# Performance work log

Measured on AMD Instinct MI355X. Metric: run time of the kernel, lower is better.

## Reference

```python
import jax, jax.numpy as jnp
import numpy as np

BS, D_HID, D_EMB, N_LABELS = 8192, 1024, 256, 64
EPS = 1e-8  # torch cosine_similarity norm clamp


def _l2norm(x):
    return x / jnp.maximum(jnp.linalg.norm(x, axis=-1, keepdims=True), EPS)


def setup_inputs() -> dict:
    key = jax.random.key(0)
    k1, k2, k3, k4 = jax.random.split(key, 4)
    return {
        "mask_emb": jax.random.normal(k1, (BS, D_HID), dtype=jnp.float32),
        "W": jax.random.normal(k2, (D_EMB, D_HID), dtype=jnp.float32) * 0.02,
        "b": jnp.zeros((D_EMB,), dtype=jnp.float32),
        "label_emb": jax.random.normal(k3, (N_LABELS, D_EMB), dtype=jnp.float32),
        "labels": jax.random.randint(k4, (BS,), 0, N_LABELS, dtype=jnp.int64 if jax.config.jax_enable_x64 else jnp.int32),
    }


def reference(mask_emb, W, b, label_emb, labels):
    bs = mask_emb.shape[0]
    emb = mask_emb @ W.T + b                      # [bs, E] transform_matrix
    en = _l2norm(emb)                              # normalized sample embeddings
    ln = _l2norm(label_emb)                        # normalized prototypes

    S = en @ en.T                                  # [bs, bs] pairwise cosine sim
    C = en @ ln.T                                  # [bs, L]  sample-vs-prototype cosine sim

    same = labels[:, None] == labels[None, :]      # [bs, bs]
    eye = jnp.eye(bs, dtype=bool)
    offdiag = ~eye

    # ---- inter-sample loss ----
    # N[i] = sum over negatives (different label) of exp(S[i,k]); constant over j
    expS = jnp.exp(S)
    N = jnp.sum(jnp.where(~same, expS, 0.0), axis=1)          # [bs]
    # pos_loss is S[i,j] for same-label j!=i, else 0
    P = jnp.where(same & offdiag, S, 0.0)                      # [bs, bs]
    terms = -P + jnp.log(N[:, None] + jnp.exp(P))
    inter = jnp.sum(jnp.where(offdiag, terms, 0.0)) / (bs * bs)

    # ---- sample-prototype losses ----
    pos = jnp.take_along_axis(C, labels[:, None], axis=1)[:, 0]   # C[i, labels[i]]
    onehot = jax.nn.one_hot(labels, label_emb.shape[0], dtype=C.dtype)
    expC = jnp.exp(C)
    neg1 = jnp.sum(expC * (1.0 - onehot), axis=1)                 # sum over other prototypes
    # neg2[i] = sum_{j: labels[j]!=labels[i]} exp(cos(label_emb[labels[i]], emb[j])) = exp(C[j, labels[i]])
    M = expC.T[labels]                                            # [bs, bs], M[i,j] = exp(C[j, labels[i]])
    neg2 = jnp.sum(jnp.where(~same, M, 0.0), axis=1)              # 0 if no negatives -> log(exp(pos)) = pos
    exp_pos = jnp.exp(pos)
    proto1 = jnp.mean(-pos + jnp.log(neg1 + exp_pos))
    proto2 = jnp.mean(-pos + jnp.log(neg2 + exp_pos))

    a1, a2 = 0.5, 0.5
    return a1 * inter + a2 * (proto1 + proto2)
```

## Files before the change

kernel.cpp:

```cpp
#include <hip/hip_runtime.h>
#include <hip/hip_bf16.h>
#include <math.h>

#define BS 8192
#define DH 1024
#define DE 256
#define NL 64
#define SBST 224

typedef __attribute__((ext_vector_type(8))) short short8;
typedef __attribute__((ext_vector_type(4))) float f32x4;
typedef unsigned short ushort;

__device__ __forceinline__ ushort bf16b(float f){
  unsigned u = __float_as_uint(f);
  unsigned r = (u + 0x7FFFu + ((u >> 16) & 1u)) >> 16;
  return (ushort)r;
}

__device__ __forceinline__ float fexp2(float x){
  float r;
  asm("v_exp_f32 %0, %1" : "=v"(r) : "v"(x));
  return r;
}

__device__ __forceinline__ void gload_lds16(const void* g, void* l){
  __builtin_amdgcn_global_load_lds((const __attribute__((address_space(1))) void*)g,
                                   (__attribute__((address_space(3))) void*)l, 16, 0, 0);
}

__global__ __launch_bounds__(256) void wcvt_kernel(const float* __restrict__ W, ushort* __restrict__ Wb){
  int i = (blockIdx.x*256 + threadIdx.x) * 8;
  float4 v0 = *(const float4*)(W+i);
  float4 v1 = *(const float4*)(W+i+4);
  short8 o;
  o[0]=bf16b(v0.x); o[1]=bf16b(v0.y); o[2]=bf16b(v0.z); o[3]=bf16b(v0.w);
  o[4]=bf16b(v1.x); o[5]=bf16b(v1.y); o[6]=bf16b(v1.z); o[7]=bf16b(v1.w);
  *(short8*)(Wb+i) = o;
}

#define EMB_AB(P) ((ushort*)pool + (P)*2048)
#define EMB_BB(P) ((ushort*)pool + 4096 + (P)*16384)

#define EMB_LOADA(KB) do { \
  va0 = *(const float4*)(aptr + (KB)); \
  va1 = *(const float4*)(aptr + (KB) + 4); \
} while(0)

#define EMB_WRITEA(P) do { \
  short8 o; \
  o[0]=bf16b(va0.x); o[1]=bf16b(va0.y); o[2]=bf16b(va0.z); o[3]=bf16b(va0.w); \
  o[4]=bf16b(va1.x); o[5]=bf16b(va1.y); o[6]=bf16b(va1.z); o[7]=bf16b(va1.w); \
  *(short8*)&EMB_AB(P)[tid*8] = o; \
} while(0)

#define EMB_STAGEB(P, KB) do { \
  _Pragma("unroll") \
  for (int q=0;q<8;q++){ \
    int chunk = q*4 + w; \
    int lin = chunk*64 + lane; \
    int row = lin >> 3, cc = lin & 7; \
    int lc = cc ^ (row & 7); \
    gload_lds16(Wb + (size_t)row*DH + (KB) + lc*8, EMB_BB(P) + chunk*512); \
  } \
} while(0)

#define EMB_COMPUTE(P) do { \
  _Pragma("unroll") \
  for (int kk=0;kk<2;kk++){ \
    short8 af[2], bfr[4]; \
    _Pragma("unroll") \
    for (int m=0;m<2;m++){ \
      int row = m*16 + (lane & 15); \
      int phys = (kk*4 + (lane >> 4)) ^ (row & 7); \
      af[m] = *(const short8*)&EMB_AB(P)[row*64 + phys*8]; \
    } \
    _Pragma("unroll") \
    for (int n=0;n<4;n++){ \
      int row = w*64 + n*16 + (lane & 15); \
      int phys = (kk*4 + (lane >> 4)) ^ (row & 7); \
      bfr[n] = *(const short8*)&EMB_BB(P)[row*64 + phys*8]; \
    } \
    _Pragma("unroll") \
    for (int m=0;m<2;m++) \
      _Pragma("unroll") \
      for (int n=0;n<4;n++) \
        acc[m][n] = __builtin_amdgcn_mfma_f32_16x16x32_bf16(af[m], bfr[n], acc[m][n], 0,0,0); \
  } \
} while(0)

__global__ __launch_bounds__(256) void emb_mega_kernel(const float* __restrict__ mask,
    const ushort* __restrict__ Wb, const float* __restrict__ bias,
    const float* __restrict__ label_emb, ushort* __restrict__ lnb,
    const int* __restrict__ labels, int* __restrict__ cnt,
    int* __restrict__ offs, int* __restrict__ groups,
    ushort* __restrict__ enb, ushort* __restrict__ enb2){
  __shared__ __align__(16) char pool[74368];
  int b = blockIdx.x, tid = threadIdx.x;
  if (b == 0){
    ushort* loc = (ushort*)pool;
    int* off_s = (int*)(pool + 32768);
    int* cnt_s = (int*)(pool + 33032);
    int t = tid;
    #pragma unroll
    for (int l=0;l<64;l++) loc[t*64 + l]=0;
    __syncthreads();
    int base = t * 32;
    for (int i=0;i<32;i++){
      int y = labels[base+i];
      loc[t*64 + y] = (ushort)(loc[t*64 + y] + 1);
    }
    __syncthreads();
    if (t < 64){
      int run = 0;
      for (int tt=0;tt<256;tt++){
        int v = loc[tt*64 + t];
        loc[tt*64 + t] = (ushort)run;
        run += v;
      }
      cnt_s[t] = run;
      cnt[t] = run;
    }
    __syncthreads();
    if (t == 0){
      int acc2 = 0;
      for (int l=0;l<64;l++){ off_s[l] = acc2; acc2 += cnt_s[l]; }
      off_s[64] = acc2;
    }
    __syncthreads();
    if (t < 65) offs[t] = off_s[t];
    for (int i=0;i<32;i++){
      int idx = base + i;
      int y = labels[idx];
      int p = off_s[y] + loc[t*64 + y];
      loc[t*64 + y] = (ushort)(loc[t*64 + y] + 1);
      groups[p] = idx;
    }
    return;
  }
  if (b < 65){
    float* red = (float*)pool;
    int l = b - 1, t = tid;
    float v = label_emb[l*DE + t];
    red[t] = v*v;
    __syncthreads();
    for (int s=128;s>0;s>>=1){
      if (t<s) red[t] += red[t+s];
      __syncthreads();
    }
    float inv = 1.0f / fmaxf(sqrtf(red[0]), 1e-8f);
    lnb[l*DE + t] = bf16b(v * inv);
    return;
  }
  float* sq = (float*)(pool + 73728);
  float* inv_s = (float*)(pool + 74240);
  int lane = tid & 63, w = tid >> 6;
  int rb = (b - 65) * 32;
  int arow = tid >> 3, alc = (tid & 7) ^ (arow & 7);
  const float* aptr = mask + (size_t)(rb + arow)*DH + alc*8;
  float4 va0, va1;
  f32x4 acc[2][4] = {};
  EMB_LOADA(0);
  EMB_WRITEA(0);
  EMB_STAGEB(0, 0);
  __syncthreads();
  int buf = 0;
  for (int kb = 0; kb < 16; kb++){
    if (kb < 15){
      EMB_LOADA((kb+1)*64);
      EMB_STAGEB(buf^1, (kb+1)*64);
    }
    EMB_COMPUTE(buf);
    if (kb < 15) EMB_WRITEA(buf^1);
    __syncthreads();
    buf ^= 1;
  }
  int qr = lane >> 4, c15 = lane & 15;
  float bv[4];
  #pragma unroll
  for (int n=0;n<4;n++) bv[n] = bias[w*64 + n*16 + c15];
  #pragma unroll
  for (int m=0;m<2;m++){
    #pragma unroll
    for (int r=0;r<4;r++){
      float s = 0.f;
      #pragma unroll
      for (int n=0;n<4;n++){
        float v = acc[m][n][r] + bv[n];
        acc[m][n][r] = v;
        s += v*v;
      }
      #pragma unroll
      for (int msk=8; msk>=1; msk>>=1) s += __shfl_xor(s, msk);
      if (c15 == 0) sq[w*32 + m*16 + qr*4 + r] = s;
    }
  }
  __syncthreads();
  if (tid < 32){
    float s = sq[tid] + sq[32+tid] + sq[64+tid] + sq[96+tid];
    inv_s[tid] = 1.0f / fmaxf(sqrtf(s), 1e-8f);
  }
  __syncthreads();
  #pragma unroll
  for (int m=0;m<2;m++){
    #pragma unroll
    for (int r=0;r<4;r++){
      int row = m*16 + qr*4 + r;
      float iv = inv_s[row];
      #pragma unroll
      for (int n=0;n<4;n++){
        int col = w*64 + n*16 + c15;
        float v = acc[m][n][r] * iv;
        enb [(size_t)(rb+row)*DE + col] = bf16b(v);
        enb2[(size_t)(rb+row)*DE + col] = bf16b(v * 1.44269504f);
      }
    }
  }
}

__global__ __launch_bounds__(256, 4) void fused3_kernel(const ushort* __restrict__ enb,
    const ushort* __restrict__ enb2, const ushort* __restrict__ lnb,
    const int* __restrict__ labels, const int* __restrict__ cnt,
    const int* __restrict__ offs, const int* __restrict__ groups,
    float* __restrict__ N_part, float* __restrict__ pos, float* __restrict__ rowsum,
    float* __restrict__ T_part, float* __restrict__ G_part,
    float* __restrict__ samesum, ushort* __restrict__ Sbuf){
  __shared__ __align__(16) char pool[33792];
  int blk = blockIdx.x;
  int tid = threadIdx.x, lane = tid & 63, w = tid >> 6;
  int qr = lane >> 4, c15 = lane & 15;

  if (blk < 128){
    ushort* Ab = (ushort*)pool;
    ushort* Bb = (ushort*)(pool + 8192);
    float* TpS = (float*)(pool + 16384);
    float* GpS = (float*)(pool + 17408);
    int rb = blk * 64;
    f32x4 acc[4] = {};
    for (int kb = 0; kb < DE; kb += 64){
      #pragma unroll
      for (int q=0;q<2;q++){
        int chunk = q*4 + w;
        int lin = chunk*64 + lane;
        int row = lin >> 3, cc = lin & 7;
        int lc = cc ^ (row & 7);
        gload_lds16(enb + (size_t)(rb+row)*DE + kb + lc*8, Ab + chunk*512);
      }
      #pragma unroll
      for (int q=0;q<2;q++){
        int chunk = q*4 + w;
        int lin = chunk*64 + lane;
        int row = lin >> 3, cc = lin & 7;
        int lc = cc ^ (row & 7);
        gload_lds16(lnb + (size_t)row*DE + kb + lc*8, Bb + chunk*512);
      }
      __syncthreads();
      #pragma unroll
      for (int kk=0;kk<2;kk++){
        int arow = w*16 + c15;
        int aphys = (kk*4 + (lane >> 4)) ^ (arow & 7);
        short8 af = *(const short8*)&Ab[arow*64 + aphys*8];
        #pragma unroll
        for (int ni=0;ni<4;ni++){
          int brow = ni*16 + c15;
          int bphys = (kk*4 + (lane >> 4)) ^ (brow & 7);
          short8 bfr = *(const short8*)&Bb[brow*64 + bphys*8];
          acc[ni] = __builtin_amdgcn_mfma_f32_16x16x32_bf16(af, bfr, acc[ni], 0,0,0);
        }
      }
      __syncthreads();
    }
    int yr[4];
    #pragma unroll
    for (int r=0;r<4;r++) yr[r] = labels[rb + w*16 + qr*4 + r];
    float e[4][4];
    #pragma unroll
    for (int ni=0;ni<4;ni++)
      #pragma unroll
      for (int r=0;r<4;r++) e[ni][r] = __expf(acc[ni][r]);
    #pragma unroll
    for (int r=0;r<4;r++){
      float rs = e[0][r]+e[1][r]+e[2][r]+e[3][r];
      float ps = 0.f;
      #pragma unroll
      for (int ni=0;ni<4;ni++) if (ni*16 + c15 == yr[r]) ps = acc[ni][r];
      #pragma unroll
      for (int msk=8; msk>=1; msk>>=1){ rs += __shfl_xor(rs, msk); ps += __shfl_xor(ps, msk); }
      if (c15 == 0){
        int grow = rb + w*16 + qr*4 + r;
        rowsum[grow] = rs;
        pos[grow] = ps;
      }
    }
    #pragma unroll
    for (int ni=0;ni<4;ni++){
      int col = ni*16 + c15;
      float t = 0.f, g = 0.f;
      #pragma unroll
      for (int r=0;r<4;r++){
        t += e[ni][r];
        if (col == yr[r]) g += e[ni][r];
      }
      t += __shfl_xor(t, 16); t += __shfl_xor(t, 32);
      g += __shfl_xor(g, 16); g += __shfl_xor(g, 32);
      if (qr == 0){ TpS[w*64 + col] = t; GpS[w*64 + col] = g; }
    }
    __syncthreads();
    if (tid < 64){
      T_part[(size_t)blk*64 + tid] = TpS[tid]+TpS[64+tid]+TpS[128+tid]+TpS[192+tid];
      G_part[(size_t)blk*64 + tid] = GpS[tid]+GpS[64+tid]+GpS[128+tid]+GpS[192+tid];
    }
    return;
  }

  if (blk < 384){
    ushort* Ab = (ushort*)pool;
    ushort* Bb = (ushort*)(pool + 8192);
    int* aidx = (int*)(pool + 24576);
    int* gidx = (int*)(pool + 24832);
    float* Gs = (float*)(pool + 25344);
    int gid = blk - 128;
    int l = gid & 63, rt = gid >> 6;
    int m = cnt[l], off = offs[l];
    ushort* Sl = Sbuf + (size_t)l * SBST * SBST;
    for (int ra = rt*64; ra < m; ra += 256){
      __syncthreads();
      if (tid < 64){ int a = ra + tid; aidx[tid] = groups[off + (a < m ? a : 0)]; }
      float Ga[4] = {0.f,0.f,0.f,0.f};
      for (int cb2 = 0; cb2 < m; cb2 += 128){
        __syncthreads();
        if (tid < 128){ int bb = cb2 + tid; gidx[tid] = groups[off + (bb < m ? bb : 0)]; }
        __syncthreads();
        f32x4 acc[4][2] = {};
        for (int kb = 0; kb < DE; kb += 64){
          #pragma unroll
          for (int q=0;q<2;q++){
            int chunk = q*4 + w;
            int lin = chunk*64 + lane;
            int row = lin >> 3, cc = lin & 7;
            int lc = cc ^ (row & 7);
            gload_lds16(enb + (size_t)aidx[row]*DE + kb + lc*8, Ab + chunk*512);
          }
          #pragma unroll
          for (int q=0;q<4;q++){
            int chunk = q*4 + w;
            int lin = chunk*64 + lane;
            int row = lin >> 3, cc = lin & 7;
            int lc = cc ^ (row & 7);
            gload_lds16(enb + (size_t)gidx[row]*DE + kb + lc*8, Bb + chunk*512);
          }
          __syncthreads();
          #pragma unroll
          for (int kk=0;kk<2;kk++){
            short8 af[4], bfr[2];
            #pragma unroll
            for (int mi=0;mi<4;mi++){
              int row = mi*16 + c15;
              int phys = (kk*4 + (lane >> 4)) ^ (row & 7);
              af[mi] = *(const short8*)&Ab[row*64 + phys*8];
            }
            #pragma unroll
            for (int ni=0;ni<2;ni++){
              int row = w*32 + ni*16 + c15;
              int phys = (kk*4 + (lane >> 4)) ^ (row & 7);
              bfr[ni] = *(const short8*)&Bb[row*64 + phys*8];
            }
            #pragma unroll
            for (int mi=0;mi<4;mi++)
              #pragma unroll
              for (int ni=0;ni<2;ni++)
                acc[mi][ni] = __builtin_amdgcn_mfma_f32_16x16x32_bf16(bfr[ni], af[mi], acc[mi][ni], 0,0,0);
          }
          __syncthreads();
        }
        #pragma unroll
        for (int mi=0;mi<4;mi++){
          int a = ra + mi*16 + c15;
          bool aok = (a < m);
          #pragma unroll
          for (int ni=0;ni<2;ni++){
            int b0 = cb2 + w*32 + ni*16 + qr*4;
            #pragma unroll
            for (int r=0;r<4;r++){
              int bb = b0 + r;
              float sv = acc[mi][ni][r];
              if (bb < m){
                Ga[mi] += __expf(sv);
                if (aok) Sl[(size_t)a*SBST + bb] = bf16b(sv);
              }
            }
          }
        }
      }
      #pragma unroll
      for (int mi=0;mi<4;mi++){
        float g = Ga[mi];
        g += __shfl_xor(g, 16);
        g += __shfl_xor(g, 32);
        if (lane < 16) Gs[w*64 + mi*16 + lane] = g;
      }
      __syncthreads();
      if (tid < 64 && ra + tid < m)
        samesum[aidx[tid]] = Gs[tid] + Gs[64+tid] + Gs[128+tid] + Gs[192+tid];
    }
    return;
  }

  ushort* Ab = (ushort*)pool;
  ushort* Bb = (ushort*)(pool + 16384);
  float* nred = (float*)(pool + 32768);
  int lin0 = blk - 384;
  int sw = (lin0 & 7) * 512 + (lin0 >> 3);
  int bx = sw & 63, by = sw >> 6;
  int wr = w >> 1, wc = w & 1;
  int rb = bx * 128;
  int cb = by * 128;
  f32x4 acc[4][4] = {};
  for (int kb = 0; kb < DE; kb += 64){
    #pragma unroll
    for (int q=0;q<4;q++){
      int chunk = q*4 + w;
      int lin2 = chunk*64 + lane;
      int row = lin2 >> 3, cc = lin2 & 7;
      int lc = cc ^ (row & 7);
      gload_lds16(enb2 + (size_t)(rb + row)*DE + kb + lc*8, Ab + chunk*512);
      gload_lds16(enb  + (size_t)(cb + row)*DE + kb + lc*8, Bb + chunk*512);
    }
    __syncthreads();
    __builtin_amdgcn_s_setprio(1);
    #pragma unroll
    for (int kk=0;kk<2;kk++){
      short8 af[4], bfr[4];
      #pragma unroll
      for (int m=0;m<4;m++){
        int row = wr*64 + m*16 + c15;
        int phys = (kk*4 + (lane >> 4)) ^ (row & 7);
        af[m] = *(const short8*)&Ab[row*64 + phys*8];
      }
      #pragma unroll
      for (int n=0;n<4;n++){
        int row = wc*64 + n*16 + c15;
        int phys = (kk*4 + (lane >> 4)) ^ (row & 7);
        bfr[n] = *(const short8*)&Bb[row*64 + phys*8];
      }
      #pragma unroll
      for (int m=0;m<4;m++)
        #pragma unroll
        for (int n=0;n<4;n++)
          acc[m][n] = __builtin_amdgcn_mfma_f32_16x16x32_bf16(bfr[n], af[m], acc[m][n], 0,0,0);
    }
    __builtin_amdgcn_s_setprio(0);
    __syncthreads();
  }
  #pragma unroll
  for (int m=0;m<4;m++){
    float s = 0.f;
    #pragma unroll
    for (int n=0;n<4;n++)
      #pragma unroll
      for (int r=0;r<4;r++)
        s += fexp2(acc[m][n][r]);
    s += __shfl_xor(s, 16);
    s += __shfl_xor(s, 32);
    if (lane < 16) nred[wc*128 + wr*64 + m*16 + lane] = s;
  }
  __syncthreads();
  if (tid < 128)
    N_part[(size_t)by * BS + rb + tid] = nred[tid] + nred[128 + tid];
}

__global__ __launch_bounds__(256) void tail_kernel(const int* __restrict__ cnt,
    const int* __restrict__ offs, const int* __restrict__ groups,
    const float* __restrict__ N_part, const float* __restrict__ samesum,
    float* __restrict__ Nrow, const ushort* __restrict__ Sbuf,
    float* __restrict__ pairp){
  __shared__ float red[256];
  __shared__ float NaS[32];
  int b = blockIdx.x, tid = threadIdx.x;
  if (b < 32){
    int i = b*256 + tid;
    float s = 0.f;
    #pragma unroll
    for (int c=0;c<64;c++) s += N_part[(size_t)c*BS + i];
    Nrow[i] = s - samesum[i];
    return;
  }
  int pid = b - 32;
  int l = pid & 63, split = pid >> 6;
  int m = cnt[l], off = offs[l];
  const ushort* Sl = Sbuf + (size_t)l * SBST * SBST;
  int r = tid >> 3, c = tid & 7;
  int a = split*32 + r;
  {
    float s0 = 0.f;
    if (a < m){
      int g = groups[off + a];
      #pragma unroll
      for (int q=0;q<8;q++) s0 += N_part[(size_t)(c + q*8)*BS + g];
    }
    #pragma unroll
    for (int msk=4; msk>=1; msk>>=1) s0 += __shfl_xor(s0, msk);
    if (c == 0 && a < m) NaS[r] = s0 - samesum[groups[off + a]];
  }
  __syncthreads();
  float sum = 0.f;
  if (a < m){
    float Na = NaS[r];
    const ushort* Srow = Sl + (size_t)a * SBST;
    int nseg = (m + 7) >> 3;
    for (int st = c; st < nseg; st += 8){
      short8 v = *(const short8*)(Srow + st*8);
      #pragma unroll
      for (int j=0;j<8;j++){
        int b2 = st*8 + j;
        if (b2 < m && b2 != a){
          float s = __uint_as_float((unsigned)(ushort)v[j] << 16);
          sum += -s + __logf(Na + __expf(s));
        }
      }
    }
  }
  red[tid] = sum;
  __syncthreads();
  for (int s=128;s>0;s>>=1){ if (tid<s) red[tid]+=red[tid+s]; __syncthreads(); }
  if (tid==0) pairp[pid] = red[0];
}

__global__ void finalize_kernel(const int* __restrict__ labels, const int* __restrict__ cnt,
    const float* __restrict__ Nrow, const float* __restrict__ pos,
    const float* __restrict__ rowsum, const float* __restrict__ T_part,
    const float* __restrict__ G_part, const float* __restrict__ pairp,
    float* __restrict__ out){
  __shared__ double red[3*256];
  __shared__ float TGp[4][64];
  __shared__ float TGf[64];
  int t = threadIdx.x;
  {
    int l = t & 63, qq = t >> 6;
    float ts = 0.f, gs = 0.f;
    for (int b=qq; b<128; b+=4){ ts += T_part[b*64 + l]; gs += G_part[b*64 + l]; }
    TGp[qq][l] = ts - gs;
  }
  __syncthreads();
  if (t < 64) TGf[t] = TGp[0][t]+TGp[1][t]+TGp[2][t]+TGp[3][t];
  __syncthreads();
  double a=0.0, p1=0.0, p2=0.0;
  for (int i=t; i<BS; i+=256){
    int y = labels[i];
    float Ni = Nrow[i];
    a += (double)((float)(BS - cnt[y]) * __logf(Ni + 1.0f));
    float ps = pos[i];
    p1 += (double)(-ps + __logf(rowsum[i]));
    p2 += (double)(-ps + __logf(TGf[y] + __expf(ps)));
  }
  red[t]=a; red[256+t]=p1; red[512+t]=p2;
  __syncthreads();
  for (int s=128;s>0;s>>=1){
    if (t<s){ red[t]+=red[t+s]; red[256+t]+=red[256+t+s]; red[512+t]+=red[512+t+s]; }
    __syncthreads();
  }
  if (t==0){
    double pair = 0.0;
    for (int l=0;l<512;l++) pair += (double)pairp[l];
    double inter = (red[0] + pair) / ((double)BS * (double)BS);
    double proto = (red[256] + red[512]) / (double)BS;
    out[0] = (float)(0.5*inter + 0.5*proto);
  }
}

extern "C" void kernel_launch(void* const* d_in, const int* in_sizes, int n_in,
                              void* d_out, int out_size, void* d_ws, size_t ws_size,
                              hipStream_t stream){
  const float* mask  = (const float*)d_in[0];
  const float* W     = (const float*)d_in[1];
  const float* bias  = (const float*)d_in[2];
  const float* lemb  = (const float*)d_in[3];
  const int*   labels= (const int*)d_in[4];
  float* out = (float*)d_out;

  ushort* enb    = (ushort*)d_ws;
  ushort* enb2   = enb + (size_t)BS*DE;
  ushort* Wb     = enb2 + (size_t)BS*DE;
  ushort* lnb    = Wb + (size_t)DE*DH;
  ushort* Sbuf   = lnb + (size_t)NL*DE;
  float*  N_part = (float*)(Sbuf + (size_t)NL*SBST*SBST);
  float*  Nrow   = N_part + (size_t)64*BS;
  float*  pos    = Nrow + BS;
  float*  rowsum = pos + BS;
  float*  samesum= rowsum + BS;
  float*  T_part = samesum + BS;
  float*  G_part = T_part + 128*64;
  float*  pairp  = G_part + 128*64;
  int* cnt    = (int*)(pairp + 512);
  int* offs   = cnt + NL;
  int* groups = offs + 68;

  hipLaunchKernelGGL(wcvt_kernel,     dim3(DE*DH/(256*8)), dim3(256), 0, stream, W, Wb);
  hipLaunchKernelGGL(emb_mega_kernel, dim3(321), dim3(256), 0, stream,
                     mask, Wb, bias, lemb, lnb, labels, cnt, offs, groups, enb, enb2);
  hipLaunchKernelGGL(fused3_kernel,   dim3(4480), dim3(256), 0, stream,
                     enb, enb2, lnb, labels, cnt, offs, groups,
                     N_part, pos, rowsum, T_part, G_part, samesum, Sbuf);
  hipLaunchKernelGGL(tail_kernel,     dim3(544), dim3(256), 0, stream,
                     cnt, offs, groups, N_part, samesum, Nrow, Sbuf, pairp);
  hipLaunchKernelGGL(finalize_kernel, dim3(1), dim3(256), 0, stream,
                     labels, cnt, Nrow, pos, rowsum, T_part, G_part, pairp, out);
}
```

Before: 128.2 us.

## Split N-pass into persistent register-A kernel with double-buffered B tiles

The all-pairs exp-sum GEMM moves out of the fused kernel into a dedicated kernel. Each block keeps a 256-row A strip in registers across the full K dimension and streams eight 64-row B tiles through double-buffered LDS, accumulating row sums in registers. This cuts redundant A reloads, per-K-step barriers and the number of N partials from 64 to 16, which also shrinks the tail reduction. It adds one kernel launch, serializes the class-group work after the N pass instead of overlapping it, and raises register pressure (launch bound of 2 blocks per unit).

```diff
diff --git a/kernel.cpp b/kernel.cpp
--- a/kernel.cpp
+++ b/kernel.cpp
@@ -218,11 +218,100 @@
   }
 }
 
-__global__ __launch_bounds__(256, 4) void fused3_kernel(const ushort* __restrict__ enb,
-    const ushort* __restrict__ enb2, const ushort* __restrict__ lnb,
-    const int* __restrict__ labels, const int* __restrict__ cnt,
-    const int* __restrict__ offs, const int* __restrict__ groups,
-    float* __restrict__ N_part, float* __restrict__ pos, float* __restrict__ rowsum,
+#define NPB_STAGE(P, J) do { \
+  _Pragma("unroll") \
+  for (int s=0; s<4; s++){ \
+    _Pragma("unroll") \
+    for (int q=0; q<2; q++){ \
+      int ck = q*4 + w; \
+      int lin = ck*64 + lane; \
+      int row = lin >> 3, cc = lin & 7; \
+      int lc = cc ^ (row & 7); \
+      gload_lds16(enb + (size_t)((J)*64 + row)*DE + s*64 + lc*8, &Bs[P][s*4096 + ck*512]); \
+    } \
+  } \
+} while(0)
+
+#define NPB_COMPUTE(P) do { \
+  f32x4 acc[4][4] = {}; \
+  _Pragma("unroll") \
+  for (int kc=0;kc<8;kc++){ \
+    int s_ = kc >> 1, kk = kc & 1; \
+    short8 bfr[4]; \
+    _Pragma("unroll") \
+    for (int n=0;n<4;n++){ \
+      int brow = n*16 + c15; \
+      int phys = (kk*4 + qr) ^ (brow & 7); \
+      bfr[n] = *(const short8*)&Bs[P][s_*4096 + brow*64 + phys*8]; \
+    } \
+    _Pragma("unroll") \
+    for (int m=0;m<4;m++) \
+      _Pragma("unroll") \
+      for (int n=0;n<4;n++) \
+        acc[m][n] = __builtin_amdgcn_mfma_f32_16x16x32_bf16(bfr[n], areg[m][kc], acc[m][n], 0,0,0); \
+  } \
+  _Pragma("unroll") \
+  for (int m=0;m<4;m++){ \
+    float s = 0.f; \
+    _Pragma("unroll") \
+    for (int n=0;n<4;n++) \
+      _Pragma("unroll") \
+      for (int r=0;r<4;r++) \
+        s += fexp2(acc[m][n][r]); \
+    srow[m] += s; \
+  } \
+} while(0)
+
+__global__ __launch_bounds__(256, 2) void npass_kernel(const ushort* __restrict__ enb,
+    const ushort* __restrict__ enb2, float* __restrict__ N_part){
+  __shared__ ushort Bs[2][16384];
+  int tid = threadIdx.x, lane = tid & 63, w = tid >> 6;
+  int qr = lane >> 4, c15 = lane & 15;
+  int bid = blockIdx.x;
+  int sw = (bid & 7) * 64 + (bid >> 3);
+  int band = sw >> 4, chunk = sw & 15;
+  int rb = band * 256;
+  int j0t = chunk * 8;
+
+  NPB_STAGE(0, j0t);
+  short8 areg[4][8];
+  #pragma unroll
+  for (int m=0;m<4;m++){
+    const ushort* ap = enb2 + (size_t)(rb + w*64 + m*16 + c15)*DE + qr*8;
+    #pragma unroll
+    for (int kc=0;kc<8;kc++)
+      areg[m][kc] = *(const short8*)(ap + kc*32);
+  }
+  float srow[4] = {0.f,0.f,0.f,0.f};
+  __syncthreads();
+
+  #pragma unroll
+  for (int t=0;t<8;t++){
+    if ((t & 1) == 0){
+      if (t < 7) NPB_STAGE(1, j0t + t + 1);
+      NPB_COMPUTE(0);
+    } else {
+      if (t < 7) NPB_STAGE(0, j0t + t + 1);
+      NPB_COMPUTE(1);
+    }
+    __syncthreads();
+  }
+
+  #pragma unroll
+  for (int m=0;m<4;m++){
+    float s = srow[m];
+    s += __shfl_xor(s, 16);
+    s += __shfl_xor(s, 32);
+    if (lane < 16)
+      N_part[(size_t)chunk*BS + rb + w*64 + m*16 + lane] = s;
+  }
+}
+
+__global__ __launch_bounds__(256, 4) void cg_kernel(const ushort* __restrict__ enb,
+    const ushort* __restrict__ lnb, const int* __restrict__ labels,
+    const int* __restrict__ cnt, const int* __restrict__ offs,
+    const int* __restrict__ groups,
+    float* __restrict__ pos, float* __restrict__ rowsum,
     float* __restrict__ T_part, float* __restrict__ G_part,
     float* __restrict__ samesum, ushort* __restrict__ Sbuf){
   __shared__ __align__(16) char pool[33792];
@@ -313,7 +402,7 @@
     return;
   }
 
-  if (blk < 384){
+  {
     ushort* Ab = (ushort*)pool;
     ushort* Bb = (ushort*)(pool + 8192);
     int* aidx = (int*)(pool + 24576);
@@ -403,70 +492,7 @@
       if (tid < 64 && ra + tid < m)
         samesum[aidx[tid]] = Gs[tid] + Gs[64+tid] + Gs[128+tid] + Gs[192+tid];
     }
-    return;
-  }
-
-  ushort* Ab = (ushort*)pool;
-  ushort* Bb = (ushort*)(pool + 16384);
-  float* nred = (float*)(pool + 32768);
-  int lin0 = blk - 384;
-  int sw = (lin0 & 7) * 512 + (lin0 >> 3);
-  int bx = sw & 63, by = sw >> 6;
-  int wr = w >> 1, wc = w & 1;
-  int rb = bx * 128;
-  int cb = by * 128;
-  f32x4 acc[4][4] = {};
-  for (int kb = 0; kb < DE; kb += 64){
-    #pragma unroll
-    for (int q=0;q<4;q++){
-      int chunk = q*4 + w;
-      int lin2 = chunk*64 + lane;
-      int row = lin2 >> 3, cc = lin2 & 7;
-      int lc = cc ^ (row & 7);
-      gload_lds16(enb2 + (size_t)(rb + row)*DE + kb + lc*8, Ab + chunk*512);
-      gload_lds16(enb  + (size_t)(cb + row)*DE + kb + lc*8, Bb + chunk*512);
-    }
-    __syncthreads();
-    __builtin_amdgcn_s_setprio(1);
-    #pragma unroll
-    for (int kk=0;kk<2;kk++){
-      short8 af[4], bfr[4];
-      #pragma unroll
-      for (int m=0;m<4;m++){
-        int row = wr*64 + m*16 + c15;
-        int phys = (kk*4 + (lane >> 4)) ^ (row & 7);
-        af[m] = *(const short8*)&Ab[row*64 + phys*8];
-      }
-      #pragma unroll
-      for (int n=0;n<4;n++){
-        int row = wc*64 + n*16 + c15;
-        int phys = (kk*4 + (lane >> 4)) ^ (row & 7);
-        bfr[n] = *(const short8*)&Bb[row*64 + phys*8];
-      }
-      #pragma unroll
-      for (int m=0;m<4;m++)
-        #pragma unroll
-        for (int n=0;n<4;n++)
-          acc[m][n] = __builtin_amdgcn_mfma_f32_16x16x32_bf16(bfr[n], af[m], acc[m][n], 0,0,0);
-    }
-    __builtin_amdgcn_s_setprio(0);
-    __syncthreads();
-  }
-  #pragma unroll
-  for (int m=0;m<4;m++){
-    float s = 0.f;
-    #pragma unroll
-    for (int n=0;n<4;n++)
-      #pragma unroll
-      for (int r=0;r<4;r++)
-        s += fexp2(acc[m][n][r]);
-    s += __shfl_xor(s, 16);
-    s += __shfl_xor(s, 32);
-    if (lane < 16) nred[wc*128 + wr*64 + m*16 + lane] = s;
-  }
-  __syncthreads();
-  if (tid < 128)
-    N_part[(size_t)by * BS + rb + tid] = nred[tid] + nred[128 + tid];
+  }
 }
 
 __global__ __launch_bounds__(256) void tail_kernel(const int* __restrict__ cnt,
@@ -481,7 +507,7 @@
     int i = b*256 + tid;
     float s = 0.f;
     #pragma unroll
-    for (int c=0;c<64;c++) s += N_part[(size_t)c*BS + i];
+    for (int c=0;c<16;c++) s += N_part[(size_t)c*BS + i];
     Nrow[i] = s - samesum[i];
     return;
   }
@@ -496,7 +522,7 @@
     if (a < m){
       int g = groups[off + a];
       #pragma unroll
-      for (int q=0;q<8;q++) s0 += N_part[(size_t)(c + q*8)*BS + g];
+      for (int q=0;q<2;q++) s0 += N_part[(size_t)(c + q*8)*BS + g];
     }
     #pragma unroll
     for (int msk=4; msk>=1; msk>>=1) s0 += __shfl_xor(s0, msk);
@@ -584,7 +610,7 @@
   ushort* lnb    = Wb + (size_t)DE*DH;
   ushort* Sbuf   = lnb + (size_t)NL*DE;
   float*  N_part = (float*)(Sbuf + (size_t)NL*SBST*SBST);
-  float*  Nrow   = N_part + (size_t)64*BS;
+  float*  Nrow   = N_part + (size_t)16*BS;
   float*  pos    = Nrow + BS;
   float*  rowsum = pos + BS;
   float*  samesum= rowsum + BS;
@@ -598,9 +624,10 @@
   hipLaunchKernelGGL(wcvt_kernel,     dim3(DE*DH/(256*8)), dim3(256), 0, stream, W, Wb);
   hipLaunchKernelGGL(emb_mega_kernel, dim3(321), dim3(256), 0, stream,
                      mask, Wb, bias, lemb, lnb, labels, cnt, offs, groups, enb, enb2);
-  hipLaunchKernelGGL(fused3_kernel,   dim3(4480), dim3(256), 0, stream,
-                     enb, enb2, lnb, labels, cnt, offs, groups,
-                     N_part, pos, rowsum, T_part, G_part, samesum, Sbuf);
+  hipLaunchKernelGGL(npass_kernel,    dim3(512), dim3(256), 0, stream, enb, enb2, N_part);
+  hipLaunchKernelGGL(cg_kernel,       dim3(384), dim3(256), 0, stream,
+                     enb, lnb, labels, cnt, offs, groups,
+                     pos, rowsum, T_part, G_part, samesum, Sbuf);
   hipLaunchKernelGGL(tail_kernel,     dim3(544), dim3(256), 0, stream,
                      cnt, offs, groups, N_part, samesum, Nrow, Sbuf, pairp);
   hipLaunchKernelGGL(finalize_kernel, dim3(1), dim3(256), 0, stream,
```

Result: slower. 151.1 us (+17.9%).

## Split prep work from embedding GEMM and widen GEMM blocks to eight waves

Applied to the files above, without the earlier changes.

Moves the W bf16 conversion, label-prototype normalization and label grouping into a single prep kernel, leaving a dedicated embedding GEMM kernel. The GEMM now uses 512 threads per block, with each wave computing a 32-column slice instead of 64. This halves per-wave accumulators and B-staging work, which should help latency hiding. In exchange, only half the threads load the A tile, and the grouping and prototype work now runs on the critical path before the GEMM instead of beside it.

```diff
diff --git a/kernel.cpp b/kernel.cpp
--- a/kernel.cpp
+++ b/kernel.cpp
@@ -29,118 +29,24 @@
                                    (__attribute__((address_space(3))) void*)l, 16, 0, 0);
 }
 
-__global__ __launch_bounds__(256) void wcvt_kernel(const float* __restrict__ W, ushort* __restrict__ Wb){
-  int i = (blockIdx.x*256 + threadIdx.x) * 8;
-  float4 v0 = *(const float4*)(W+i);
-  float4 v1 = *(const float4*)(W+i+4);
-  short8 o;
-  o[0]=bf16b(v0.x); o[1]=bf16b(v0.y); o[2]=bf16b(v0.z); o[3]=bf16b(v0.w);
-  o[4]=bf16b(v1.x); o[5]=bf16b(v1.y); o[6]=bf16b(v1.z); o[7]=bf16b(v1.w);
-  *(short8*)(Wb+i) = o;
-}
-
-#define EMB_AB(P) ((ushort*)pool + (P)*2048)
-#define EMB_BB(P) ((ushort*)pool + 4096 + (P)*16384)
-
-#define EMB_LOADA(KB) do { \
-  va0 = *(const float4*)(aptr + (KB)); \
-  va1 = *(const float4*)(aptr + (KB) + 4); \
-} while(0)
-
-#define EMB_WRITEA(P) do { \
-  short8 o; \
-  o[0]=bf16b(va0.x); o[1]=bf16b(va0.y); o[2]=bf16b(va0.z); o[3]=bf16b(va0.w); \
-  o[4]=bf16b(va1.x); o[5]=bf16b(va1.y); o[6]=bf16b(va1.z); o[7]=bf16b(va1.w); \
-  *(short8*)&EMB_AB(P)[tid*8] = o; \
-} while(0)
-
-#define EMB_STAGEB(P, KB) do { \
-  _Pragma("unroll") \
-  for (int q=0;q<8;q++){ \
-    int chunk = q*4 + w; \
-    int lin = chunk*64 + lane; \
-    int row = lin >> 3, cc = lin & 7; \
-    int lc = cc ^ (row & 7); \
-    gload_lds16(Wb + (size_t)row*DH + (KB) + lc*8, EMB_BB(P) + chunk*512); \
-  } \
-} while(0)
-
-#define EMB_COMPUTE(P) do { \
-  _Pragma("unroll") \
-  for (int kk=0;kk<2;kk++){ \
-    short8 af[2], bfr[4]; \
-    _Pragma("unroll") \
-    for (int m=0;m<2;m++){ \
-      int row = m*16 + (lane & 15); \
-      int phys = (kk*4 + (lane >> 4)) ^ (row & 7); \
-      af[m] = *(const short8*)&EMB_AB(P)[row*64 + phys*8]; \
-    } \
-    _Pragma("unroll") \
-    for (int n=0;n<4;n++){ \
-      int row = w*64 + n*16 + (lane & 15); \
-      int phys = (kk*4 + (lane >> 4)) ^ (row & 7); \
-      bfr[n] = *(const short8*)&EMB_BB(P)[row*64 + phys*8]; \
-    } \
-    _Pragma("unroll") \
-    for (int m=0;m<2;m++) \
-      _Pragma("unroll") \
-      for (int n=0;n<4;n++) \
-        acc[m][n] = __builtin_amdgcn_mfma_f32_16x16x32_bf16(af[m], bfr[n], acc[m][n], 0,0,0); \
-  } \
-} while(0)
-
-__global__ __launch_bounds__(256) void emb_mega_kernel(const float* __restrict__ mask,
-    const ushort* __restrict__ Wb, const float* __restrict__ bias,
+__global__ __launch_bounds__(256) void prep_kernel(const float* __restrict__ W, ushort* __restrict__ Wb,
     const float* __restrict__ label_emb, ushort* __restrict__ lnb,
     const int* __restrict__ labels, int* __restrict__ cnt,
-    int* __restrict__ offs, int* __restrict__ groups,
-    ushort* __restrict__ enb, ushort* __restrict__ enb2){
-  __shared__ __align__(16) char pool[74368];
-  int b = blockIdx.x, tid = threadIdx.x;
-  if (b == 0){
-    ushort* loc = (ushort*)pool;
-    int* off_s = (int*)(pool + 32768);
-    int* cnt_s = (int*)(pool + 33032);
-    int t = tid;
-    #pragma unroll
-    for (int l=0;l<64;l++) loc[t*64 + l]=0;
-    __syncthreads();
-    int base = t * 32;
-    for (int i=0;i<32;i++){
-      int y = labels[base+i];
-      loc[t*64 + y] = (ushort)(loc[t*64 + y] + 1);
-    }
-    __syncthreads();
-    if (t < 64){
-      int run = 0;
-      for (int tt=0;tt<256;tt++){
-        int v = loc[tt*64 + t];
-        loc[tt*64 + t] = (ushort)run;
-        run += v;
-      }
-      cnt_s[t] = run;
-      cnt[t] = run;
-    }
-    __syncthreads();
-    if (t == 0){
-      int acc2 = 0;
-      for (int l=0;l<64;l++){ off_s[l] = acc2; acc2 += cnt_s[l]; }
-      off_s[64] = acc2;
-    }
-    __syncthreads();
-    if (t < 65) offs[t] = off_s[t];
-    for (int i=0;i<32;i++){
-      int idx = base + i;
-      int y = labels[idx];
-      int p = off_s[y] + loc[t*64 + y];
-      loc[t*64 + y] = (ushort)(loc[t*64 + y] + 1);
-      groups[p] = idx;
-    }
+    int* __restrict__ offs, int* __restrict__ groups){
+  int b = blockIdx.x, t = threadIdx.x;
+  if (b < 128){
+    int i = (b*256 + t) * 8;
+    float4 v0 = *(const float4*)(W+i);
+    float4 v1 = *(const float4*)(W+i+4);
+    short8 o;
+    o[0]=bf16b(v0.x); o[1]=bf16b(v0.y); o[2]=bf16b(v0.z); o[3]=bf16b(v0.w);
+    o[4]=bf16b(v1.x); o[5]=bf16b(v1.y); o[6]=bf16b(v1.z); o[7]=bf16b(v1.w);
+    *(short8*)(Wb+i) = o;
     return;
   }
-  if (b < 65){
-    float* red = (float*)pool;
-    int l = b - 1, t = tid;
+  if (b < 192){
+    __shared__ float red[256];
+    int l = b - 128;
     float v = label_emb[l*DE + t];
     red[t] = v*v;
     __syncthreads();
@@ -152,14 +58,110 @@
     lnb[l*DE + t] = bf16b(v * inv);
     return;
   }
-  float* sq = (float*)(pool + 73728);
-  float* inv_s = (float*)(pool + 74240);
-  int lane = tid & 63, w = tid >> 6;
-  int rb = (b - 65) * 32;
+  __shared__ ushort loc[256][64];
+  __shared__ int off_s[65];
+  __shared__ int cnt_s[64];
+  #pragma unroll
+  for (int l=0;l<64;l++) loc[t][l]=0;
+  __syncthreads();
+  int base = t * 32;
+  for (int i=0;i<32;i++){
+    int y = labels[base+i];
+    loc[t][y] = (ushort)(loc[t][y] + 1);
+  }
+  __syncthreads();
+  if (t < 64){
+    int run = 0;
+    for (int tt=0;tt<256;tt++){
+      int v = loc[tt][t];
+      loc[tt][t] = (ushort)run;
+      run += v;
+    }
+    cnt_s[t] = run;
+    cnt[t] = run;
+  }
+  __syncthreads();
+  if (t == 0){
+    int acc = 0;
+    for (int l=0;l<64;l++){ off_s[l] = acc; acc += cnt_s[l]; }
+    off_s[64] = acc;
+  }
+  __syncthreads();
+  if (t < 65) offs[t] = off_s[t];
+  for (int i=0;i<32;i++){
+    int idx = base + i;
+    int y = labels[idx];
+    int p = off_s[y] + loc[t][y];
+    loc[t][y] = (ushort)(loc[t][y] + 1);
+    groups[p] = idx;
+  }
+}
+
+#define EMB_LOADA(KB) do { \
+  if (tid < 256){ \
+    va0 = *(const float4*)(aptr + (KB)); \
+    va1 = *(const float4*)(aptr + (KB) + 4); \
+  } \
+} while(0)
+
+#define EMB_WRITEA(P) do { \
+  if (tid < 256){ \
+    short8 o; \
+    o[0]=bf16b(va0.x); o[1]=bf16b(va0.y); o[2]=bf16b(va0.z); o[3]=bf16b(va0.w); \
+    o[4]=bf16b(va1.x); o[5]=bf16b(va1.y); o[6]=bf16b(va1.z); o[7]=bf16b(va1.w); \
+    *(short8*)&Ab[P][tid*8] = o; \
+  } \
+} while(0)
+
+#define EMB_STAGEB(P, KB) do { \
+  _Pragma("unroll") \
+  for (int q=0;q<4;q++){ \
+    int chunk = q*8 + w; \
+    int lin = chunk*64 + lane; \
+    int row = lin >> 3, cc = lin & 7; \
+    int lc = cc ^ (row & 7); \
+    gload_lds16(Wb + (size_t)row*DH + (KB) + lc*8, Bb[P] + chunk*512); \
+  } \
+} while(0)
+
+#define EMB_COMPUTE(P) do { \
+  _Pragma("unroll") \
+  for (int kk=0;kk<2;kk++){ \
+    short8 af[2], bfr[2]; \
+    _Pragma("unroll") \
+    for (int m=0;m<2;m++){ \
+      int row = m*16 + c15; \
+      int phys = (kk*4 + qr) ^ (row & 7); \
+      af[m] = *(const short8*)&Ab[P][row*64 + phys*8]; \
+    } \
+    _Pragma("unroll") \
+    for (int n=0;n<2;n++){ \
+      int row = w*32 + n*16 + c15; \
+      int phys = (kk*4 + qr) ^ (row & 7); \
+      bfr[n] = *(const short8*)&Bb[P][row*64 + phys*8]; \
+    } \
+    _Pragma("unroll") \
+    for (int m=0;m<2;m++) \
+      _Pragma("unroll") \
+      for (int n=0;n<2;n++) \
+        acc[m][n] = __builtin_amdgcn_mfma_f32_16x16x32_bf16(af[m], bfr[n], acc[m][n], 0,0,0); \
+  } \
+} while(0)
+
+__global__ __launch_bounds__(512) void emb_kernel(const float* __restrict__ mask,
+    const ushort* __restrict__ Wb, const float* __restrict__ bias,
+    ushort* __restrict__ enb, ushort* __restrict__ enb2){
+  __shared__ ushort Ab[2][32*64];
+  __shared__ ushort Bb[2][256*64];
+  __shared__ float sq[8][32];
+  __shared__ float inv_s[32];
+  int tid = threadIdx.x, lane = tid & 63, w = tid >> 6;
+  int qr = lane >> 4, c15 = lane & 15;
+  int rb = blockIdx.x * 32;
   int arow = tid >> 3, alc = (tid & 7) ^ (arow & 7);
-  const float* aptr = mask + (size_t)(rb + arow)*DH + alc*8;
+  const float* aptr = mask + (size_t)(rb + (arow & 31))*DH + alc*8;
   float4 va0, va1;
-  f32x4 acc[2][4] = {};
+  f32x4 acc[2][2] = {};
   EMB_LOADA(0);
   EMB_WRITEA(0);
   EMB_STAGEB(0, 0);
@@ -175,29 +177,30 @@
     __syncthreads();
     buf ^= 1;
   }
-  int qr = lane >> 4, c15 = lane & 15;
-  float bv[4];
+  float bv[2];
   #pragma unroll
-  for (int n=0;n<4;n++) bv[n] = bias[w*64 + n*16 + c15];
+  for (int n=0;n<2;n++) bv[n] = bias[w*32 + n*16 + c15];
   #pragma unroll
   for (int m=0;m<2;m++){
     #pragma unroll
     for (int r=0;r<4;r++){
       float s = 0.f;
       #pragma unroll
-      for (int n=0;n<4;n++){
+      for (int n=0;n<2;n++){
         float v = acc[m][n][r] + bv[n];
         acc[m][n][r] = v;
         s += v*v;
       }
       #pragma unroll
       for (int msk=8; msk>=1; msk>>=1) s += __shfl_xor(s, msk);
-      if (c15 == 0) sq[w*32 + m*16 + qr*4 + r] = s;
+      if (c15 == 0) sq[w][m*16 + qr*4 + r] = s;
     }
   }
   __syncthreads();
   if (tid < 32){
-    float s = sq[tid] + sq[32+tid] + sq[64+tid] + sq[96+tid];
+    float s = 0.f;
+    #pragma unroll
+    for (int q=0;q<8;q++) s += sq[q][tid];
     inv_s[tid] = 1.0f / fmaxf(sqrtf(s), 1e-8f);
   }
   __syncthreads();
@@ -208,8 +211,8 @@
       int row = m*16 + qr*4 + r;
       float iv = inv_s[row];
       #pragma unroll
-      for (int n=0;n<4;n++){
-        int col = w*64 + n*16 + c15;
+      for (int n=0;n<2;n++){
+        int col = w*32 + n*16 + c15;
         float v = acc[m][n][r] * iv;
         enb [(size_t)(rb+row)*DE + col] = bf16b(v);
         enb2[(size_t)(rb+row)*DE + col] = bf16b(v * 1.44269504f);
@@ -595,9 +598,8 @@
   int* offs   = cnt + NL;
   int* groups = offs + 68;
 
-  hipLaunchKernelGGL(wcvt_kernel,     dim3(DE*DH/(256*8)), dim3(256), 0, stream, W, Wb);
-  hipLaunchKernelGGL(emb_mega_kernel, dim3(321), dim3(256), 0, stream,
-                     mask, Wb, bias, lemb, lnb, labels, cnt, offs, groups, enb, enb2);
+  hipLaunchKernelGGL(prep_kernel,     dim3(193), dim3(256), 0, stream, W, Wb, lemb, lnb, labels, cnt, offs, groups);
+  hipLaunchKernelGGL(emb_kernel,      dim3(BS/32), dim3(512), 0, stream, mask, Wb, bias, enb, enb2);
   hipLaunchKernelGGL(fused3_kernel,   dim3(4480), dim3(256), 0, stream,
                      enb, enb2, lnb, labels, cnt, offs, groups,
                      N_part, pos, rowsum, T_part, G_part, samesum, Sbuf);
```

Result: no change. 126.6 us (-1.3%).
